# Optimization experiments

Hardware: AMD Instinct MI355X
Metric: run time of the kernel (lower is better)

## Reference

```python
import jax, jax.numpy as jnp
import numpy as np

B, S, D, H = 4, 1024, 512, 8
EPS = 1e-5


def _cx(x):
    # [..., 2] float -> complex
    return jax.lax.complex(x[..., 0], x[..., 1])


def setup_inputs() -> dict:
    key = jax.random.key(0)
    ks = jax.random.split(key, 9)
    f = lambda k, sh: jax.random.normal(k, sh, dtype=jnp.float32)
    inp = {
        "q": f(ks[0], (B, S, D, 2)),
        "k": f(ks[1], (B, S, D, 2)),
        "v": f(ks[2], (B, S, D, 2)),
        "Wq": f(ks[3], (D, D, 2)) * 0.02,
        "bq": f(ks[4], (D, 2)) * 0.02,
        "Wk": f(ks[5], (D, D, 2)) * 0.02,
        "bk": f(ks[6], (D, 2)) * 0.02,
        "Wv": f(ks[7], (D, D, 2)) * 0.02,
        "bv": f(ks[8], (D, 2)) * 0.02,
        "gamma_r": jnp.ones((D,), jnp.float32),
        "beta_r": jnp.zeros((D,), jnp.float32),
        "gamma_i": jnp.ones((D,), jnp.float32),
        "beta_i": jnp.zeros((D,), jnp.float32),
        "n_heads": H,
    }
    return inp


def _layernorm(x, g, b):
    # torch LayerNorm: biased variance, eps inside sqrt
    mu = jnp.mean(x, axis=-1, keepdims=True)
    var = jnp.mean((x - mu) ** 2, axis=-1, keepdims=True)
    return (x - mu) / jnp.sqrt(var + EPS) * g + b


def reference(q, k, v, Wq, bq, Wk, bk, Wv, bv, gamma_r, beta_r, gamma_i, beta_i, n_heads):
    qc, kc, vc = _cx(q), _cx(k), _cx(v)
    # complex linear: x @ W^T + b
    Q = jnp.einsum("bsd,ed->bse", qc, _cx(Wq)) + _cx(bq)
    K = jnp.einsum("bsd,ed->bse", kc, _cx(Wk)) + _cx(bk)
    V = jnp.einsum("bsd,ed->bse", vc, _cx(Wv)) + _cx(bv)
    b, s, d = qc.shape
    dh = d // n_heads
    Qh = Q.reshape(b, s, n_heads, dh)
    Kh = K.reshape(b, s, n_heads, dh)
    Vh = V.reshape(b, s, n_heads, dh)
    # complex scores [b,h,q,k], scaled by sqrt(dh)
    scores = jnp.einsum("bqhd,bkhd->bhqk", Qh, Kh) / jnp.sqrt(jnp.float32(dh))
    # original: softmax over view_as_real dim=-2 == key axis, real & imag independently
    attn = jax.lax.complex(jax.nn.softmax(scores.real, axis=-1),
                           jax.nn.softmax(scores.imag, axis=-1))
    # (dropout is identity in eval mode)
    out = jnp.einsum("bhqk,bkhd->bqhd", attn, Vh).reshape(b, s, d)
    out = out + qc  # residual
    out_r = _layernorm(out.real, gamma_r, beta_r)
    out_i = _layernorm(out.imag, gamma_i, beta_i)
    return jnp.stack([out_r, out_i], axis=-1)  # [B,S,D,2]
```

## Files before the change

kernel.cpp:

```cpp
#include <hip/hip_runtime.h>
#include <math.h>

#define BB  4
#define SS  1024
#define DD  512
#define HH  8
#define DHD 64
#define PL  2097152
#define WPL 262144

constexpr float LN_EPS = 1e-5f;

using half4 = __attribute__((ext_vector_type(4))) _Float16;
using half8 = __attribute__((ext_vector_type(8))) _Float16;
using f32x4 = __attribute__((ext_vector_type(4))) float;

__device__ __forceinline__ half8 negh(half8 a) {
    union { half8 h; unsigned int u[4]; } t;
    t.h = a;
    #pragma unroll
    for (int i = 0; i < 4; ++i) t.u[i] ^= 0x80008000u;
    return t.h;
}
__device__ __forceinline__ half8 ldh64(const unsigned short* p, int row, int col) {
    return *(const half8*)(p + row * 64 + (col ^ ((row & 7) << 3)));
}
#define MFMA16(acc, a, b) acc = __builtin_amdgcn_mfma_f32_16x16x32_f16(a, b, acc, 0, 0, 0)

__global__ __launch_bounds__(256)
void cvt_kernel(const float2* __restrict__ s0, const float2* __restrict__ s1,
                const float2* __restrict__ s2, unsigned short* __restrict__ dst,
                int planeElems) {
    const int z = blockIdx.y;
    const float2* src = z == 0 ? s0 : (z == 1 ? s1 : s2);
    unsigned short* base = dst + (size_t)z * 2 * planeElems;
    const int idx = (blockIdx.x * 256 + threadIdx.x) * 2;
    float4 t = *(const float4*)(src + idx);
    union { _Float16 h[2]; unsigned int u; } r, i;
    r.h[0] = (_Float16)t.x; r.h[1] = (_Float16)t.z;
    i.h[0] = (_Float16)t.y; i.h[1] = (_Float16)t.w;
    ((unsigned int*)(base))[idx >> 1] = r.u;
    ((unsigned int*)(base + planeElems))[idx >> 1] = i.u;
}

__global__ __launch_bounds__(256, 5)
void proj_kernel(const unsigned short* __restrict__ XP,
                 const unsigned short* __restrict__ WP,
                 const float2* __restrict__ bq, const float2* __restrict__ bk,
                 const float2* __restrict__ bv,
                 unsigned short* __restrict__ QG, unsigned short* __restrict__ KG,
                 unsigned short* __restrict__ VG) {
    const unsigned short* XR = XP + (size_t)blockIdx.z * 2 * PL;
    const unsigned short* XI = XR + PL;
    const unsigned short* WR = WP + (size_t)blockIdx.z * 2 * WPL;
    const unsigned short* WI = WR + WPL;
    const float2* bias; unsigned short* outP;
    if (blockIdx.z == 0)      { bias = bq; outP = QG; }
    else if (blockIdx.z == 1) { bias = bk; outP = KG; }
    else                      { bias = bv; outP = VG; }
    const bool isV = (blockIdx.z == 2);

    __shared__ unsigned short Xs[2][4096];
    __shared__ unsigned short Ws[2][4096];

    const int tid  = threadIdx.x;
    const int w    = tid >> 6;
    const int lane = tid & 63;
    const int quad = lane >> 4;
    const int l15  = lane & 15;
    const int m0   = blockIdx.x * 64;
    const int h    = blockIdx.y;
    const int e0   = h * 64;

    const int r8 = tid >> 3;
    const int g8 = tid & 7;

    f32x4 Sr[4], Si[4];
    #pragma unroll
    for (int i = 0; i < 4; ++i) { Sr[i] = (f32x4)0.f; Si[i] = (f32x4)0.f; }

    for (int dc = 0; dc < DD; dc += 64) {
        if (dc) __syncthreads();
        #pragma unroll
        for (int it = 0; it < 2; ++it) {
            const int row = it * 32 + r8;
            const int off = row * 64 + ((g8 ^ (row & 7)) << 3);
            const size_t xo = (size_t)(m0 + row) * DD + dc + g8 * 8;
            const size_t wo = (size_t)(e0 + row) * DD + dc + g8 * 8;
            *(uint4*)&Xs[0][off] = *(const uint4*)(XR + xo);
            *(uint4*)&Xs[1][off] = *(const uint4*)(XI + xo);
            *(uint4*)&Ws[0][off] = *(const uint4*)(WR + wo);
            *(uint4*)&Ws[1][off] = *(const uint4*)(WI + wo);
        }
        __syncthreads();

        const int mrow = w * 16 + l15;
        #pragma unroll
        for (int kc = 0; kc < 2; ++kc) {
            const int dl = kc * 32 + quad * 8;
            half8 xr  = ldh64(Xs[0], mrow, dl);
            half8 xi  = ldh64(Xs[1], mrow, dl);
            half8 xmi = negh(xi);
            #pragma unroll
            for (int et = 0; et < 4; ++et) {
                const int er = et * 16 + l15;
                half8 wr = ldh64(Ws[0], er, dl);
                half8 wi = ldh64(Ws[1], er, dl);
                MFMA16(Sr[et], xr,  wr);
                MFMA16(Sr[et], xmi, wi);
                MFMA16(Si[et], xr,  wi);
                MFMA16(Si[et], xi,  wr);
            }
        }
    }

    #pragma unroll
    for (int et = 0; et < 4; ++et) {
        const int col = et * 16 + l15;
        float2 bb = bias[e0 + col];
        #pragma unroll
        for (int reg = 0; reg < 4; ++reg) {
            int m = m0 + w * 16 + quad * 4 + reg;
            int b = m >> 10;
            int s = m & 1023;
            int bh = b * HH + h;
            union { _Float16 h; unsigned short u; } cr, ci;
            cr.h = (_Float16)(Sr[et][reg] + bb.x);
            ci.h = (_Float16)(Si[et][reg] + bb.y);
            size_t o = isV ? ((size_t)bh * DHD + col) * SS + s
                           : ((size_t)bh * SS + s) * DHD + col;
            outP[0 * PL + o] = cr.u;
            outP[1 * PL + o] = ci.u;
        }
    }
}

#define AWID 72
__global__ __launch_bounds__(256, 2)
void attn_kernel(const unsigned short* __restrict__ QG, const unsigned short* __restrict__ KG,
                 const unsigned short* __restrict__ VG,
                 unsigned short* __restrict__ ObR, unsigned short* __restrict__ ObI) {
    __shared__ unsigned short Ks[2][64 * AWID];
    __shared__ unsigned short Vt[2][64 * AWID];
    __shared__ unsigned short Ps[2][64 * AWID];
    __shared__ float lbuf[2][2][64];

    const int n   = blockIdx.x;
    const int bh  = (n & 7) * 4 + (n >> 7);
    const int q0  = ((n >> 3) & 15) * 64;
    const int b   = bh >> 3;
    const int h   = bh & 7;

    const int tid  = threadIdx.x;
    const int w    = tid >> 6;
    const int lane = tid & 63;
    const int quad = lane >> 4;
    const int l15  = lane & 15;
    const int sw   = w & 1;
    const int tw   = w >> 1;

    half8 qfr[2][2], qfi[2][2], qfmi[2][2];
    #pragma unroll
    for (int qt = 0; qt < 2; ++qt)
        #pragma unroll
        for (int kc = 0; kc < 2; ++kc) {
            size_t qa = ((size_t)bh * SS + q0 + sw * 32 + qt * 16 + l15) * DHD + kc * 32 + quad * 8;
            qfr[qt][kc]  = *(const half8*)(QG + qa);
            qfi[qt][kc]  = *(const half8*)(QG + PL + qa);
            qfmi[qt][kc] = negh(qfi[qt][kc]);
        }

    f32x4 acc[2][2][4];
    #pragma unroll
    for (int qt = 0; qt < 2; ++qt)
        #pragma unroll
        for (int dt = 0; dt < 2; ++dt)
            #pragma unroll
            for (int p = 0; p < 4; ++p) acc[qt][dt][p] = (f32x4)0.f;
    float lacc[2][2] = {{0.f, 0.f}, {0.f, 0.f}};

    const int srow = tid >> 3;
    const int sg   = (tid & 7) * 8;

    for (int kt = 0; kt < SS; kt += 64) {
        __syncthreads();
        #pragma unroll
        for (int p = 0; p < 2; ++p)
            #pragma unroll
            for (int it = 0; it < 2; ++it) {
                const int r = it * 32 + srow;
                *(uint4*)&Ks[p][r * AWID + sg] =
                    *(const uint4*)(KG + (size_t)p * PL + ((size_t)bh * SS + kt + r) * DHD + sg);
                *(uint4*)&Vt[p][r * AWID + sg] =
                    *(const uint4*)(VG + (size_t)p * PL + ((size_t)bh * DHD + r) * SS + kt + sg);
            }
        __syncthreads();

        f32x4 Sr[2][2], Si[2][2];
        #pragma unroll
        for (int a = 0; a < 2; ++a)
            #pragma unroll
            for (int c = 0; c < 2; ++c) { Sr[a][c] = (f32x4)0.f; Si[a][c] = (f32x4)0.f; }
        #pragma unroll
        for (int kc = 0; kc < 2; ++kc) {
            #pragma unroll
            for (int kt2 = 0; kt2 < 2; ++kt2) {
                const int krow = tw * 32 + kt2 * 16 + l15;
                half8 akr = *(const half8*)&Ks[0][krow * AWID + kc * 32 + quad * 8];
                half8 aki = *(const half8*)&Ks[1][krow * AWID + kc * 32 + quad * 8];
                #pragma unroll
                for (int qt = 0; qt < 2; ++qt) {
                    MFMA16(Sr[kt2][qt], akr, qfr[qt][kc]);
                    MFMA16(Sr[kt2][qt], aki, qfmi[qt][kc]);
                    MFMA16(Si[kt2][qt], aki, qfr[qt][kc]);
                    MFMA16(Si[kt2][qt], akr, qfi[qt][kc]);
                }
            }
        }

        #pragma unroll
        for (int kt2 = 0; kt2 < 2; ++kt2)
            #pragma unroll
            for (int qt = 0; qt < 2; ++qt) {
                half4 pr, pi;
                float sr_ = 0.f, si_ = 0.f;
                #pragma unroll
                for (int reg = 0; reg < 4; ++reg) {
                    float er = __expf(Sr[kt2][qt][reg] * 0.125f);
                    float ei = __expf(Si[kt2][qt][reg] * 0.125f);
                    pr[reg] = (_Float16)er;
                    pi[reg] = (_Float16)ei;
                    sr_ += (float)pr[reg];
                    si_ += (float)pi[reg];
                }
                lacc[qt][0] += sr_;
                lacc[qt][1] += si_;
                const int qrow = sw * 32 + qt * 16 + l15;
                const int kcol = tw * 32 + kt2 * 16 + quad * 4;
                *(half4*)&Ps[0][qrow * AWID + kcol] = pr;
                *(half4*)&Ps[1][qrow * AWID + kcol] = pi;
            }
        __syncthreads();

        #pragma unroll
        for (int kc = 0; kc < 2; ++kc) {
            half8 ap[2][2];
            #pragma unroll
            for (int qt = 0; qt < 2; ++qt) {
                const int qrow = sw * 32 + qt * 16 + l15;
                ap[qt][0] = *(const half8*)&Ps[0][qrow * AWID + kc * 32 + quad * 8];
                ap[qt][1] = *(const half8*)&Ps[1][qrow * AWID + kc * 32 + quad * 8];
            }
            #pragma unroll
            for (int dt = 0; dt < 2; ++dt) {
                const int drow = tw * 32 + dt * 16 + l15;
                half8 bvr = *(const half8*)&Vt[0][drow * AWID + kc * 32 + quad * 8];
                half8 bvi = *(const half8*)&Vt[1][drow * AWID + kc * 32 + quad * 8];
                #pragma unroll
                for (int qt = 0; qt < 2; ++qt) {
                    MFMA16(acc[qt][dt][0], ap[qt][0], bvr);
                    MFMA16(acc[qt][dt][1], ap[qt][0], bvi);
                    MFMA16(acc[qt][dt][2], ap[qt][1], bvr);
                    MFMA16(acc[qt][dt][3], ap[qt][1], bvi);
                }
            }
        }
    }

    __syncthreads();
    #pragma unroll
    for (int qt = 0; qt < 2; ++qt)
        #pragma unroll
        for (int p = 0; p < 2; ++p) {
            float v = lacc[qt][p];
            v += __shfl_xor(v, 16);
            v += __shfl_xor(v, 32);
            if (lane < 16) lbuf[p][tw][sw * 32 + qt * 16 + lane] = v;
        }
    __syncthreads();

    #pragma unroll
    for (int qt = 0; qt < 2; ++qt)
        #pragma unroll
        for (int reg = 0; reg < 4; ++reg) {
            const int qloc = sw * 32 + qt * 16 + quad * 4 + reg;
            const float ir = 1.f / (lbuf[0][0][qloc] + lbuf[0][1][qloc]);
            const float ii = 1.f / (lbuf[1][0][qloc] + lbuf[1][1][qloc]);
            #pragma unroll
            for (int dt = 0; dt < 2; ++dt) {
                const int d = tw * 32 + dt * 16 + l15;
                union { _Float16 h; unsigned short u; } cr, ci;
                cr.h = (_Float16)(acc[qt][dt][0][reg] * ir - acc[qt][dt][3][reg] * ii);
                ci.h = (_Float16)(acc[qt][dt][1][reg] * ir + acc[qt][dt][2][reg] * ii);
                size_t o = ((size_t)b * SS + q0 + qloc) * DD + h * DHD + d;
                ObR[o] = cr.u;
                ObI[o] = ci.u;
            }
        }
}

__global__ __launch_bounds__(256)
void ln_kernel(const unsigned short* __restrict__ OrP, const unsigned short* __restrict__ OiP,
               const float2* __restrict__ Qin,
               const float* __restrict__ gr, const float* __restrict__ br,
               const float* __restrict__ gi, const float* __restrict__ bi,
               float2* __restrict__ out) {
    const int row = blockIdx.x;
    const int tid = threadIdx.x;
    const size_t base = (size_t)row * DD;
    const int e0 = 2 * tid, e1 = 2 * tid + 1;

    union { unsigned int u; _Float16 h[2]; } tr, ti;
    tr.u = *(const unsigned int*)(OrP + base + e0);
    ti.u = *(const unsigned int*)(OiP + base + e0);
    float2 r0 = Qin[base + e0];
    float2 r1 = Qin[base + e1];
    float xr0 = (float)tr.h[0] + r0.x;
    float xr1 = (float)tr.h[1] + r1.x;
    float xi0 = (float)ti.h[0] + r0.y;
    float xi1 = (float)ti.h[1] + r1.y;

    float sr = xr0 + xr1;
    float si = xi0 + xi1;
    float qr = xr0 * xr0 + xr1 * xr1;
    float qi = xi0 * xi0 + xi1 * xi1;
    #pragma unroll
    for (int off = 32; off > 0; off >>= 1) {
        sr += __shfl_down(sr, off);
        si += __shfl_down(si, off);
        qr += __shfl_down(qr, off);
        qi += __shfl_down(qi, off);
    }
    __shared__ float red[4][4];
    __shared__ float stat[4];
    int lane = tid & 63, wid = tid >> 6;
    if (lane == 0) { red[wid][0] = sr; red[wid][1] = si; red[wid][2] = qr; red[wid][3] = qi; }
    __syncthreads();
    if (tid == 0) {
        sr = red[0][0] + red[1][0] + red[2][0] + red[3][0];
        si = red[0][1] + red[1][1] + red[2][1] + red[3][1];
        qr = red[0][2] + red[1][2] + red[2][2] + red[3][2];
        qi = red[0][3] + red[1][3] + red[2][3] + red[3][3];
        float mur = sr * (1.f / DD), mui = si * (1.f / DD);
        float vr = qr * (1.f / DD) - mur * mur;
        float vi = qi * (1.f / DD) - mui * mui;
        stat[0] = mur; stat[1] = mui;
        stat[2] = rsqrtf(vr + LN_EPS); stat[3] = rsqrtf(vi + LN_EPS);
    }
    __syncthreads();
    float mur = stat[0], mui = stat[1], rsr = stat[2], rsi = stat[3];
    out[base + e0] = make_float2((xr0 - mur) * rsr * gr[e0] + br[e0],
                                 (xi0 - mui) * rsi * gi[e0] + bi[e0]);
    out[base + e1] = make_float2((xr1 - mur) * rsr * gr[e1] + br[e1],
                                 (xi1 - mui) * rsi * gi[e1] + bi[e1]);
}

extern "C" void kernel_launch(void* const* d_in, const int* in_sizes, int n_in,
                              void* d_out, int out_size, void* d_ws, size_t ws_size,
                              hipStream_t stream) {
    const float2* q  = (const float2*)d_in[0];
    const float2* k  = (const float2*)d_in[1];
    const float2* v  = (const float2*)d_in[2];
    const float2* Wq = (const float2*)d_in[3];
    const float2* bq = (const float2*)d_in[4];
    const float2* Wk = (const float2*)d_in[5];
    const float2* bk = (const float2*)d_in[6];
    const float2* Wv = (const float2*)d_in[7];
    const float2* bv = (const float2*)d_in[8];
    const float*  gr = (const float*)d_in[9];
    const float*  br = (const float*)d_in[10];
    const float*  gi = (const float*)d_in[11];
    const float*  bi = (const float*)d_in[12];

    unsigned short* XP  = (unsigned short*)d_ws;
    unsigned short* WP  = XP + (size_t)6 * PL;
    unsigned short* QG  = WP + (size_t)6 * WPL;
    unsigned short* KG  = QG + (size_t)2 * PL;
    unsigned short* VG  = KG + (size_t)2 * PL;
    unsigned short* ObR = VG + (size_t)2 * PL;
    unsigned short* ObI = ObR + (size_t)PL;

    cvt_kernel<<<dim3(4096, 3), 256, 0, stream>>>(q, k, v, XP, PL);
    cvt_kernel<<<dim3(512, 3), 256, 0, stream>>>(Wq, Wk, Wv, WP, WPL);
    proj_kernel<<<dim3(64, 8, 3), 256, 0, stream>>>(XP, WP, bq, bk, bv, QG, KG, VG);
    attn_kernel<<<dim3(512), 256, 0, stream>>>(QG, KG, VG, ObR, ObI);
    ln_kernel<<<dim3(BB * SS), 256, 0, stream>>>(ObR, ObI, q, gr, br, gi, bi, (float2*)d_out);
}
```

Measured before the change: 224.7 us.

## Fuse fp32-to-fp16 split conversion into projection kernel loads

Removes the two standalone conversion kernels and has the projection kernel read the interleaved fp32 complex inputs and weights directly, converting to split real/imag fp16 planes while staging into shared memory. This drops a full write and re-read of the fp16 copies of the activations and two kernel launches. The warp tiling also changes from 16x64 per wave to a 2x2 arrangement of 32x32 sub-tiles, which cuts redundant shared-memory loads per MFMA. The cost is that each projection block reads twice the bytes in fp32, and weights are re-converted by every block; occupancy hint drops from 5 to 4.

Result: slower. 268.0 us (+19.3%).

```diff
diff --git a/kernel.cpp b/kernel.cpp
--- a/kernel.cpp
+++ b/kernel.cpp
@@ -7,7 +7,6 @@
 #define HH  8
 #define DHD 64
 #define PL  2097152
-#define WPL 262144
 
 constexpr float LN_EPS = 1e-5f;
 
@@ -27,37 +26,19 @@
 }
 #define MFMA16(acc, a, b) acc = __builtin_amdgcn_mfma_f32_16x16x32_f16(a, b, acc, 0, 0, 0)
 
-__global__ __launch_bounds__(256)
-void cvt_kernel(const float2* __restrict__ s0, const float2* __restrict__ s1,
-                const float2* __restrict__ s2, unsigned short* __restrict__ dst,
-                int planeElems) {
-    const int z = blockIdx.y;
-    const float2* src = z == 0 ? s0 : (z == 1 ? s1 : s2);
-    unsigned short* base = dst + (size_t)z * 2 * planeElems;
-    const int idx = (blockIdx.x * 256 + threadIdx.x) * 2;
-    float4 t = *(const float4*)(src + idx);
-    union { _Float16 h[2]; unsigned int u; } r, i;
-    r.h[0] = (_Float16)t.x; r.h[1] = (_Float16)t.z;
-    i.h[0] = (_Float16)t.y; i.h[1] = (_Float16)t.w;
-    ((unsigned int*)(base))[idx >> 1] = r.u;
-    ((unsigned int*)(base + planeElems))[idx >> 1] = i.u;
-}
-
-__global__ __launch_bounds__(256, 5)
-void proj_kernel(const unsigned short* __restrict__ XP,
-                 const unsigned short* __restrict__ WP,
+__global__ __launch_bounds__(256, 4)
+void proj_kernel(const float2* __restrict__ qin, const float2* __restrict__ kin,
+                 const float2* __restrict__ vin,
+                 const float2* __restrict__ Wq, const float2* __restrict__ Wk,
+                 const float2* __restrict__ Wv,
                  const float2* __restrict__ bq, const float2* __restrict__ bk,
                  const float2* __restrict__ bv,
                  unsigned short* __restrict__ QG, unsigned short* __restrict__ KG,
                  unsigned short* __restrict__ VG) {
-    const unsigned short* XR = XP + (size_t)blockIdx.z * 2 * PL;
-    const unsigned short* XI = XR + PL;
-    const unsigned short* WR = WP + (size_t)blockIdx.z * 2 * WPL;
-    const unsigned short* WI = WR + WPL;
-    const float2* bias; unsigned short* outP;
-    if (blockIdx.z == 0)      { bias = bq; outP = QG; }
-    else if (blockIdx.z == 1) { bias = bk; outP = KG; }
-    else                      { bias = bv; outP = VG; }
+    const float2* X; const float2* W; const float2* bias; unsigned short* outP;
+    if (blockIdx.z == 0)      { X = qin; W = Wq; bias = bq; outP = QG; }
+    else if (blockIdx.z == 1) { X = kin; W = Wk; bias = bk; outP = KG; }
+    else                      { X = vin; W = Wv; bias = bv; outP = VG; }
     const bool isV = (blockIdx.z == 2);
 
     __shared__ unsigned short Xs[2][4096];
@@ -71,68 +52,99 @@
     const int m0   = blockIdx.x * 64;
     const int h    = blockIdx.y;
     const int e0   = h * 64;
-
-    const int r8 = tid >> 3;
-    const int g8 = tid & 7;
-
-    f32x4 Sr[4], Si[4];
-    #pragma unroll
-    for (int i = 0; i < 4; ++i) { Sr[i] = (f32x4)0.f; Si[i] = (f32x4)0.f; }
+    const int sw   = w & 1;
+    const int tw   = w >> 1;
+
+    const int srow = tid >> 2;
+    const int sc   = (tid & 3) * 16;
+    const int ga   = sc >> 3;
+    const int go0  = srow * 64 + ((ga ^ (srow & 7)) << 3);
+    const int go1  = srow * 64 + (((ga + 1) ^ (srow & 7)) << 3);
+
+    f32x4 Sr[2][2], Si[2][2];
+    #pragma unroll
+    for (int a = 0; a < 2; ++a)
+        #pragma unroll
+        for (int c = 0; c < 2; ++c) { Sr[a][c] = (f32x4)0.f; Si[a][c] = (f32x4)0.f; }
 
     for (int dc = 0; dc < DD; dc += 64) {
         if (dc) __syncthreads();
-        #pragma unroll
-        for (int it = 0; it < 2; ++it) {
-            const int row = it * 32 + r8;
-            const int off = row * 64 + ((g8 ^ (row & 7)) << 3);
-            const size_t xo = (size_t)(m0 + row) * DD + dc + g8 * 8;
-            const size_t wo = (size_t)(e0 + row) * DD + dc + g8 * 8;
-            *(uint4*)&Xs[0][off] = *(const uint4*)(XR + xo);
-            *(uint4*)&Xs[1][off] = *(const uint4*)(XI + xo);
-            *(uint4*)&Ws[0][off] = *(const uint4*)(WR + wo);
-            *(uint4*)&Ws[1][off] = *(const uint4*)(WI + wo);
+        {
+            const float4* xp = (const float4*)(X + (size_t)(m0 + srow) * DD + dc + sc);
+            union { _Float16 h[16]; uint4 q[2]; } hr, hi;
+            #pragma unroll
+            for (int j = 0; j < 8; ++j) {
+                float4 t = xp[j];
+                hr.h[2*j]   = (_Float16)t.x; hi.h[2*j]   = (_Float16)t.y;
+                hr.h[2*j+1] = (_Float16)t.z; hi.h[2*j+1] = (_Float16)t.w;
+            }
+            *(uint4*)&Xs[0][go0] = hr.q[0]; *(uint4*)&Xs[0][go1] = hr.q[1];
+            *(uint4*)&Xs[1][go0] = hi.q[0]; *(uint4*)&Xs[1][go1] = hi.q[1];
+        }
+        {
+            const float4* wp = (const float4*)(W + (size_t)(e0 + srow) * DD + dc + sc);
+            union { _Float16 h[16]; uint4 q[2]; } hr, hi;
+            #pragma unroll
+            for (int j = 0; j < 8; ++j) {
+                float4 t = wp[j];
+                hr.h[2*j]   = (_Float16)t.x; hi.h[2*j]   = (_Float16)t.y;
+                hr.h[2*j+1] = (_Float16)t.z; hi.h[2*j+1] = (_Float16)t.w;
+            }
+            *(uint4*)&Ws[0][go0] = hr.q[0]; *(uint4*)&Ws[0][go1] = hr.q[1];
+            *(uint4*)&Ws[1][go0] = hi.q[0]; *(uint4*)&Ws[1][go1] = hi.q[1];
         }
         __syncthreads();
 
-        const int mrow = w * 16 + l15;
         #pragma unroll
         for (int kc = 0; kc < 2; ++kc) {
             const int dl = kc * 32 + quad * 8;
-            half8 xr  = ldh64(Xs[0], mrow, dl);
-            half8 xi  = ldh64(Xs[1], mrow, dl);
-            half8 xmi = negh(xi);
-            #pragma unroll
-            for (int et = 0; et < 4; ++et) {
-                const int er = et * 16 + l15;
-                half8 wr = ldh64(Ws[0], er, dl);
-                half8 wi = ldh64(Ws[1], er, dl);
-                MFMA16(Sr[et], xr,  wr);
-                MFMA16(Sr[et], xmi, wi);
-                MFMA16(Si[et], xr,  wi);
-                MFMA16(Si[et], xi,  wr);
-            }
+            half8 xr[2], xi[2], xmi[2], wr[2], wi[2];
+            #pragma unroll
+            for (int mt = 0; mt < 2; ++mt) {
+                const int mrow = sw * 32 + mt * 16 + l15;
+                xr[mt]  = ldh64(Xs[0], mrow, dl);
+                xi[mt]  = ldh64(Xs[1], mrow, dl);
+                xmi[mt] = negh(xi[mt]);
+            }
+            #pragma unroll
+            for (int et = 0; et < 2; ++et) {
+                const int er = tw * 32 + et * 16 + l15;
+                wr[et] = ldh64(Ws[0], er, dl);
+                wi[et] = ldh64(Ws[1], er, dl);
+            }
+            #pragma unroll
+            for (int mt = 0; mt < 2; ++mt)
+                #pragma unroll
+                for (int et = 0; et < 2; ++et) {
+                    MFMA16(Sr[mt][et], xr[mt],  wr[et]);
+                    MFMA16(Sr[mt][et], xmi[mt], wi[et]);
+                    MFMA16(Si[mt][et], xr[mt],  wi[et]);
+                    MFMA16(Si[mt][et], xi[mt],  wr[et]);
+                }
         }
     }
 
     #pragma unroll
-    for (int et = 0; et < 4; ++et) {
-        const int col = et * 16 + l15;
-        float2 bb = bias[e0 + col];
-        #pragma unroll
-        for (int reg = 0; reg < 4; ++reg) {
-            int m = m0 + w * 16 + quad * 4 + reg;
-            int b = m >> 10;
-            int s = m & 1023;
-            int bh = b * HH + h;
-            union { _Float16 h; unsigned short u; } cr, ci;
-            cr.h = (_Float16)(Sr[et][reg] + bb.x);
-            ci.h = (_Float16)(Si[et][reg] + bb.y);
-            size_t o = isV ? ((size_t)bh * DHD + col) * SS + s
-                           : ((size_t)bh * SS + s) * DHD + col;
-            outP[0 * PL + o] = cr.u;
-            outP[1 * PL + o] = ci.u;
-        }
-    }
+    for (int mt = 0; mt < 2; ++mt)
+        #pragma unroll
+        for (int et = 0; et < 2; ++et) {
+            const int col = tw * 32 + et * 16 + l15;
+            float2 bb = bias[e0 + col];
+            #pragma unroll
+            for (int reg = 0; reg < 4; ++reg) {
+                int m = m0 + sw * 32 + mt * 16 + quad * 4 + reg;
+                int b = m >> 10;
+                int s = m & 1023;
+                int bh = b * HH + h;
+                union { _Float16 h; unsigned short u; } cr, ci;
+                cr.h = (_Float16)(Sr[mt][et][reg] + bb.x);
+                ci.h = (_Float16)(Si[mt][et][reg] + bb.y);
+                size_t o = isV ? ((size_t)bh * DHD + col) * SS + s
+                               : ((size_t)bh * SS + s) * DHD + col;
+                outP[0 * PL + o] = cr.u;
+                outP[1 * PL + o] = ci.u;
+            }
+        }
 }
 
 #define AWID 72
@@ -372,17 +384,13 @@
     const float*  gi = (const float*)d_in[11];
     const float*  bi = (const float*)d_in[12];
 
-    unsigned short* XP  = (unsigned short*)d_ws;
-    unsigned short* WP  = XP + (size_t)6 * PL;
-    unsigned short* QG  = WP + (size_t)6 * WPL;
+    unsigned short* QG  = (unsigned short*)d_ws;
     unsigned short* KG  = QG + (size_t)2 * PL;
     unsigned short* VG  = KG + (size_t)2 * PL;
     unsigned short* ObR = VG + (size_t)2 * PL;
     unsigned short* ObI = ObR + (size_t)PL;
 
-    cvt_kernel<<<dim3(4096, 3), 256, 0, stream>>>(q, k, v, XP, PL);
-    cvt_kernel<<<dim3(512, 3), 256, 0, stream>>>(Wq, Wk, Wv, WP, WPL);
-    proj_kernel<<<dim3(64, 8, 3), 256, 0, stream>>>(XP, WP, bq, bk, bv, QG, KG, VG);
+    proj_kernel<<<dim3(64, 8, 3), 256, 0, stream>>>(q, k, v, Wq, Wk, Wv, bq, bk, bv, QG, KG, VG);
     attn_kernel<<<dim3(512), 256, 0, stream>>>(QG, KG, VG, ObR, ObI);
     ln_kernel<<<dim3(BB * SS), 256, 0, stream>>>(ObR, ObI, q, gr, br, gi, bi, (float2*)d_out);
 }
```
